# Optimization experiments

Hardware: AMD Instinct MI355X
Metric: run time of the kernel (lower is better)

Reference implementation:

```python
import jax, jax.numpy as jnp
import numpy as np

B, C_IN, N_NODES = 128, 64, 1024
N_TRIPLES = 3 * (N_NODES - 1)  # node 0 is the shared zero vector


def _btc(x, idx, w, b):
    # x: [B, C, N]; idx: [B, 3M]; w: [O, C, 3]; b: [O]
    Bv, C, _ = x.shape
    T = idx.shape[1]
    g = jnp.take_along_axis(x, jnp.broadcast_to(idx[:, None, :], (Bv, C, T)), axis=2)
    g = g.reshape(Bv, C, T // 3, 3)  # stride-3 kernel-3 conv == per-triple contraction
    out = jnp.einsum('bcnk,ock->bon', g, w) + b[None, :, None]
    zero = jnp.zeros((Bv, out.shape[1], 1), dtype=out.dtype)
    return jnp.concatenate([zero, out], axis=2)  # re-prepend zero node -> [B, O, N]


def _tln(x):
    mean = jnp.mean(x, axis=(1, 2), keepdims=True)
    std = jnp.std(x, axis=(1, 2), ddof=1, keepdims=True)  # torch.std is unbiased
    return (x - mean) / (std + 1e-5)


def _tower(x, idx, p):
    x = jax.nn.leaky_relu(_tln(_btc(x, idx, p['w_conv1'], p['b_conv1'])), 0.01)
    x = jax.nn.leaky_relu(_tln(_btc(x, idx, p['w_conv2'], p['b_conv2'])), 0.01)
    x = _tln(_btc(x, idx, p['w_conv3'], p['b_conv3']))
    x = jnp.max(x, axis=2)  # DynamicPooling -> [B, 64]
    x = jax.nn.leaky_relu(x @ p['w_fc1'].T + p['b_fc1'], 0.01)
    return x @ p['w_fc2'].T + p['b_fc2']  # [B, 1]  (Dropout is identity at eval)


def setup_inputs() -> dict:
    key = jax.random.key(0)
    ks = jax.random.split(key, 12)
    s = 0.05
    return {
        'data1': jax.random.normal(ks[0], (B, C_IN, N_NODES), jnp.float32),
        'idx1': jax.random.randint(ks[1], (B, N_TRIPLES, 1), 0, N_NODES, dtype=jnp.int64)
                if jax.config.jax_enable_x64 else
                jax.random.randint(ks[1], (B, N_TRIPLES, 1), 0, N_NODES).astype(jnp.int32),
        'data2': jax.random.normal(ks[2], (B, C_IN, N_NODES), jnp.float32),
        'idx2': jax.random.randint(ks[3], (B, N_TRIPLES, 1), 0, N_NODES).astype(jnp.int32),
        'w_conv1': jax.random.normal(ks[4], (256, C_IN, 3), jnp.float32) * s,
        'b_conv1': jnp.zeros((256,), jnp.float32),
        'w_conv2': jax.random.normal(ks[5], (128, 256, 3), jnp.float32) * s,
        'b_conv2': jnp.zeros((128,), jnp.float32),
        'w_conv3': jax.random.normal(ks[6], (64, 128, 3), jnp.float32) * s,
        'b_conv3': jnp.zeros((64,), jnp.float32),
        'w_fc1': jax.random.normal(ks[7], (32, 64), jnp.float32) * s,
        'b_fc1': jnp.zeros((32,), jnp.float32),
        'w_fc2': jax.random.normal(ks[8], (1, 32), jnp.float32) * s,
        'b_fc2': jnp.zeros((1,), jnp.float32),
    }


def reference(data1, idx1, data2, idx2,
              w_conv1, b_conv1, w_conv2, b_conv2, w_conv3, b_conv3,
              w_fc1, b_fc1, w_fc2, b_fc2):
    p = dict(w_conv1=w_conv1, b_conv1=b_conv1, w_conv2=w_conv2, b_conv2=b_conv2,
             w_conv3=w_conv3, b_conv3=b_conv3, w_fc1=w_fc1, b_fc1=b_fc1,
             w_fc2=w_fc2, b_fc2=b_fc2)
    y1 = _tower(data1, idx1[..., 0], p)
    y2 = _tower(data2, idx2[..., 0], p)
    return jnp.squeeze(jax.nn.sigmoid(y1 - y2), axis=1)  # [B]
```

## Files before the change

### kernel.cpp

```cpp
#include <hip/hip_runtime.h>
#include <math.h>

typedef __attribute__((ext_vector_type(8))) short short8;
typedef __attribute__((ext_vector_type(4))) float f32x4;
typedef __attribute__((ext_vector_type(2))) float f32x2;

#define LRELU(x) ((x) > 0.0f ? (x) : 0.01f * (x))

struct __align__(4) Int3 { int x, y, z; };

__device__ __forceinline__ unsigned short f2bf(float f) {
    unsigned int u = __float_as_uint(f);
    return (unsigned short)((u + 0x7FFFu + ((u >> 16) & 1u)) >> 16);
}
__device__ __forceinline__ unsigned int pack_bf16_pair(float lo, float hi) {
    unsigned int ul = __float_as_uint(lo) + 0x8000u;
    unsigned int uh = __float_as_uint(hi) + 0x8000u;
    return (ul >> 16) | (uh & 0xFFFF0000u);
}
__device__ __forceinline__ float2 stats_from(const float* sums, int b, float count) {
    float s = sums[2 * b], q = sums[2 * b + 1];
    float mean = s / count;
    float var = (q - s * s / count) / (count - 1.0f);
    var = fmaxf(var, 0.0f);
    return make_float2(mean, 1.0f / (sqrtf(var) + 1e-5f));
}
__device__ __forceinline__ void atomicMaxF(float* a, float v) {
    if (v >= 0.0f) atomicMax((int*)a, __float_as_int(v));
    else           atomicMin((unsigned int*)a, __float_as_uint(v));
}
__device__ __forceinline__ unsigned int fp8x4_nact(unsigned int u, float a, float c) {
    f32x2 lo = __builtin_amdgcn_cvt_pk_f32_fp8(u, false);
    f32x2 hi = __builtin_amdgcn_cvt_pk_f32_fp8(u, true);
    lo = lo * a + c; hi = hi * a + c;
    f32x2 ml = lo * 0.01f, mh = hi * 0.01f;
    lo = __builtin_elementwise_max(lo, ml);
    hi = __builtin_elementwise_max(hi, mh);
    int r = __builtin_amdgcn_cvt_pk_fp8_f32(lo.x, lo.y, 0, false);
    r = __builtin_amdgcn_cvt_pk_fp8_f32(hi.x, hi.y, r, true);
    return (unsigned int)r;
}
__device__ __forceinline__ int perm128(int o) {
    return ((o >> 6) << 6) | (((o >> 3) & 3) << 4) | (((o >> 5) & 1) << 3) | (o & 7);
}

template <int MT, int WM>
__device__ __forceinline__ void mfma_step(const unsigned short* wt, const unsigned short* gt,
                                          f32x4 (&acc)[MT][4],
                                          int wo, int wn, int quad, int l15, int blkid)
{
#pragma unroll
    for (int st = 0; st < 2; ++st) {
        short8 af[MT], bfv[4];
        const int qb = st * 4 + quad;
#pragma unroll
        for (int i = 0; i < MT; i++) {
            const int orow = wo * WM + i * 16 + l15;
            af[i] = *(const short8*)&wt[orow * 64 + ((qb ^ blkid) << 3)];
        }
#pragma unroll
        for (int t = 0; t < 4; t++) {
            const int nrow = wn * 64 + t * 16 + l15;
            bfv[t] = *(const short8*)&gt[nrow * 64 + ((qb ^ blkid) << 3)];
        }
#pragma unroll
        for (int i = 0; i < MT; i++)
#pragma unroll
            for (int t = 0; t < 4; t++)
                acc[i][t] = __builtin_amdgcn_mfma_f32_16x16x32_bf16(
                    af[i], bfv[t], acc[i][t], 0, 0, 0);
    }
}

__global__ void prep_all(const float* __restrict__ w1, unsigned short* __restrict__ wq1,
                         const float* __restrict__ w2, unsigned char* __restrict__ wq2,
                         const float* __restrict__ w3, unsigned char* __restrict__ wq3)
{
    const int tid = blockIdx.x * blockDim.x + threadIdx.x;
    const int stride = gridDim.x * blockDim.x;
    for (int i = tid; i < 256 * 192; i += stride) {
        int o = i / 192, kp = i - o * 192;
        int j = kp >> 6, c = kp & 63;
        wq1[i] = f2bf(w1[(o * 64 + c) * 3 + j]);
    }
    for (int i = tid; i < (128 * 768) >> 2; i += stride) {
        const int e0 = i << 2;
        const int o = e0 / 768, r0 = e0 - o * 768;
        const int kc = r0 >> 7, ro = r0 & 127;
        const int k0 = ((ro >> 6) << 6) + (((ro >> 3) & 1) << 5) + (((ro >> 4) & 3) << 3) + (ro & 7);
        const int kp0 = kc * 128 + k0;
        const int j = kp0 >> 8, c0 = kp0 & 255;
        const float* src = &w2[(o * 256 + c0) * 3 + j];
        float f0 = src[0], f1 = src[3], f2 = src[6], f3 = src[9];
        int r = __builtin_amdgcn_cvt_pk_fp8_f32(f0, f1, 0, false);
        r = __builtin_amdgcn_cvt_pk_fp8_f32(f2, f3, r, true);
        *(unsigned int*)&wq2[e0] = (unsigned int)r;
    }
    for (int i = tid; i < (64 * 384) >> 2; i += stride) {
        const int e0 = i << 2;
        const int o = e0 / 384, r0 = e0 - o * 384;
        const int kc = r0 >> 7, ro = r0 & 127;
        const int k0 = ((ro >> 6) << 6) + (((ro >> 3) & 1) << 5) + (((ro >> 4) & 3) << 3) + (ro & 7);
        const int kp0 = kc * 128 + k0;
        const int j = kp0 >> 7, c0 = kp0 & 127;
        const float* src = &w3[(o * 128 + c0) * 3 + j];
        float f0 = src[0], f1 = src[3], f2 = src[6], f3 = src[9];
        int r = __builtin_amdgcn_cvt_pk_fp8_f32(f0, f1, 0, false);
        r = __builtin_amdgcn_cvt_pk_fp8_f32(f2, f3, r, true);
        *(unsigned int*)&wq3[e0] = (unsigned int)r;
    }
}

__global__ __launch_bounds__(256) void transpose_in(const float* __restrict__ inA,
                                                    const float* __restrict__ inB,
                                                    unsigned short* __restrict__ xT,
                                                    float* __restrict__ sums,
                                                    unsigned int* __restrict__ pmax)
{
    const int b = blockIdx.y, n0 = blockIdx.x * 64;
    const float* in = (b >= 128 ? inB : inA) + ((size_t)(b & 127) * 64) * 1024;
    const int tid = threadIdx.x;
    if (blockIdx.x == 0 && blockIdx.y == 0) {
        const int nBv = gridDim.y;
        for (int i = tid; i < 3 * nBv * 2; i += 256) sums[i] = 0.0f;
        for (int i = tid; i < nBv * 64; i += 256) pmax[i] = 0xFFFFFFFFu;
    }
    __shared__ float tile[64][65];
    const int nn = tid & 63, cw = tid >> 6;
#pragma unroll
    for (int i = 0; i < 16; i++) {
        int c = i * 4 + cw;
        tile[c][nn] = in[(size_t)c * 1024 + n0 + nn];
    }
    __syncthreads();
    const int n = tid >> 2, cp = (tid & 3) * 16;
    unsigned int pk[8];
#pragma unroll
    for (int i = 0; i < 8; i++) {
        unsigned short lo = f2bf(tile[cp + 2 * i][n]);
        unsigned short hi = f2bf(tile[cp + 2 * i + 1][n]);
        pk[i] = (unsigned int)lo | ((unsigned int)hi << 16);
    }
    unsigned short* dst = xT + ((size_t)b * 1024 + n0 + n) * 64 + cp;
    uint4 v0 = {pk[0], pk[1], pk[2], pk[3]};
    uint4 v1 = {pk[4], pk[5], pk[6], pk[7]};
    *(uint4*)dst = v0;
    *(uint4*)(dst + 8) = v1;
}

__global__ __launch_bounds__(256) void norm_act_fp8(unsigned char* __restrict__ a,
                                                    const float* __restrict__ sums,
                                                    float count, int u4PerB)
{
    const int b = blockIdx.y;
    float2 st = stats_from(sums, b, count);
    const float na = st.y, nc = -st.x * st.y;
    uint4* p = (uint4*)a + (size_t)b * u4PerB;
    for (int idx = blockIdx.x * 256 + threadIdx.x; idx < u4PerB; idx += gridDim.x * 256) {
        uint4 v = p[idx];
        v.x = fp8x4_nact(v.x, na, nc);
        v.y = fp8x4_nact(v.y, na, nc);
        v.z = fp8x4_nact(v.z, na, nc);
        v.w = fp8x4_nact(v.w, na, nc);
        p[idx] = v;
    }
}

__global__ __launch_bounds__(256, 3) void conv1_mfma(
    const unsigned short* __restrict__ xT,
    const int* __restrict__ idxA,
    const int* __restrict__ idxB,
    const unsigned short* __restrict__ wq,
    const float* __restrict__ bias,
    unsigned char* __restrict__ out,
    float* __restrict__ sums)
{
    const int b   = blockIdx.x;
    const int o0  = blockIdx.y * 128;
    const int nt0 = blockIdx.z << 7;
    const int tid = threadIdx.x;
    const int lane = tid & 63, wave = tid >> 6;
    const int wo = wave & 1, wn = wave >> 1;
    const int quad = lane >> 4, l15 = lane & 15;
    const int blkid = lane & 7;

    __shared__ __align__(16) unsigned short wt[128 * 64];
    __shared__ __align__(16) unsigned short gt[128 * 64];

    f32x4 acc[4][4];
#pragma unroll
    for (int i = 0; i < 4; i++)
#pragma unroll
        for (int t = 0; t < 4; t++) acc[i][t] = (f32x4){0.f, 0.f, 0.f, 0.f};

    const unsigned short* xTb = xT + (((size_t)b) << 10) * 64;
    const int* idxb = (b >= 128 ? idxB : idxA) + (size_t)(b & 127) * 3069;

    const int gr = tid >> 1, gh = tid & 1;
    int s0, s1, s2;
    {
        int n = nt0 + gr;
        int t0 = (n == 0) ? 0 : (n - 1);
        const Int3 sv = *(const Int3*)&idxb[3 * t0];
        s0 = sv.x; s1 = sv.y; s2 = sv.z;
    }
    const int wr = tid >> 1, wseg = tid & 1;
    const unsigned short* wrow = wq + (size_t)(o0 + wr) * 192 + wseg * 32;
    const int gswz = gr & 7, wswz = wr & 7;

    uint4 g0A, g1A, g2A, g3A;
    uint4 g0B, g1B, g2B, g3B;

#define LOADC(S, KC) {                                                           \
        const int src_ = ((KC) == 0) ? s0 : (((KC) == 1) ? s1 : s2);             \
        const uint4* gp_ = (const uint4*)(xTb + (size_t)src_ * 64 + gh * 32);    \
        g0##S = gp_[0]; g1##S = gp_[1]; g2##S = gp_[2]; g3##S = gp_[3];          \
    }

#define STAGE(S, KC) {                                                           \
        const uint4* wp_ = (const uint4*)(wrow + ((KC) << 6));                   \
        uint4 wv0 = wp_[0], wv1 = wp_[1], wv2 = wp_[2], wv3 = wp_[3];            \
        *(uint4*)&gt[gr * 64 + (((gh << 2) | 0) ^ gswz) * 8] = g0##S;            \
        *(uint4*)&gt[gr * 64 + (((gh << 2) | 1) ^ gswz) * 8] = g1##S;            \
        *(uint4*)&gt[gr * 64 + (((gh << 2) | 2) ^ gswz) * 8] = g2##S;            \
        *(uint4*)&gt[gr * 64 + (((gh << 2) | 3) ^ gswz) * 8] = g3##S;            \
        *(uint4*)&wt[wr * 64 + ((wseg * 4 + 0) ^ wswz) * 8] = wv0;               \
        *(uint4*)&wt[wr * 64 + ((wseg * 4 + 1) ^ wswz) * 8] = wv1;               \
        *(uint4*)&wt[wr * 64 + ((wseg * 4 + 2) ^ wswz) * 8] = wv2;               \
        *(uint4*)&wt[wr * 64 + ((wseg * 4 + 3) ^ wswz) * 8] = wv3;               \
    }

    LOADC(A, 0);
    LOADC(B, 1);
    int kc = 0;
    for (; kc + 2 <= 3; kc += 2) {
        if (kc) __syncthreads();
        STAGE(A, kc);
        if (kc + 2 < 3) LOADC(A, kc + 2);
        __syncthreads();
        mfma_step<4, 64>(wt, gt, acc, wo, wn, quad, l15, blkid);
        __syncthreads();
        STAGE(B, kc + 1);
        __syncthreads();
        mfma_step<4, 64>(wt, gt, acc, wo, wn, quad, l15, blkid);
    }
    {
        __syncthreads();
        STAGE(A, 2);
        __syncthreads();
        mfma_step<4, 64>(wt, gt, acc, wo, wn, quad, l15, blkid);
    }
#undef LOADC
#undef STAGE

    __syncthreads();
    unsigned char* eb = (unsigned char*)gt;
    float lsum = 0.f, lsq = 0.f;
#pragma unroll
    for (int i = 0; i < 4; i++) {
        const int obl = wo * 64 + i * 16 + quad * 4;
        const int op  = perm128(obl);
        const float4 bv = *(const float4*)(bias + o0 + obl);
#pragma unroll
        for (int t = 0; t < 4; t++) {
            const int nl = wn * 64 + t * 16 + l15;
            float v0 = acc[i][t][0] + bv.x;
            float v1 = acc[i][t][1] + bv.y;
            float v2 = acc[i][t][2] + bv.z;
            float v3 = acc[i][t][3] + bv.w;
            if (nt0 + nl == 0) { v0 = v1 = v2 = v3 = 0.f; }
            lsum += v0 + v1 + v2 + v3;
            lsq  += v0 * v0 + v1 * v1 + v2 * v2 + v3 * v3;
            int r = __builtin_amdgcn_cvt_pk_fp8_f32(v0, v1, 0, false);
            r = __builtin_amdgcn_cvt_pk_fp8_f32(v2, v3, r, true);
            *(unsigned int*)&eb[nl * 128 + (op ^ ((nl & 7) << 4))] = (unsigned int)r;
        }
    }
#pragma unroll
    for (int off = 32; off > 0; off >>= 1) {
        lsum += __shfl_down(lsum, off);
        lsq  += __shfl_down(lsq, off);
    }
    float* red = (float*)wt;
    if (lane == 0) { red[wave] = lsum; red[4 + wave] = lsq; }
    __syncthreads();
#pragma unroll
    for (int c = 0; c < 4; ++c) {
        const int ch = c * 256 + tid;
        const int row = ch >> 3, off = (ch & 7) << 4;
        uint4 v = *(const uint4*)&eb[row * 128 + (off ^ ((row & 7) << 4))];
        *(uint4*)&out[((size_t)b * 1024 + nt0 + row) * 256 + o0 + off] = v;
    }
    if (tid == 0) {
        atomicAdd(&sums[2 * b + 0], red[0] + red[1] + red[2] + red[3]);
        atomicAdd(&sums[2 * b + 1], red[4] + red[5] + red[6] + red[7]);
    }
}

__global__ __launch_bounds__(256, 3) void conv2_fp8(
    const unsigned char* __restrict__ a1,
    const int* __restrict__ idxA,
    const int* __restrict__ idxB,
    const unsigned char* __restrict__ wq8,
    const float* __restrict__ bias,
    unsigned char* __restrict__ out,
    float* __restrict__ sums)
{
    const int b   = blockIdx.x;
    const int nt0 = blockIdx.z << 7;
    const int tid = threadIdx.x;
    const int lane = tid & 63, wave = tid >> 6;
    const int wo = wave & 1, wn = wave >> 1;
    const int quad = lane >> 4, l15 = lane & 15;
    const int blkid = lane & 7;

    __shared__ __align__(16) unsigned char wt8[128 * 128];
    __shared__ __align__(16) unsigned char gt8[128 * 128];

    f32x4 acc[4][4];
#pragma unroll
    for (int i = 0; i < 4; i++)
#pragma unroll
        for (int t = 0; t < 4; t++) acc[i][t] = (f32x4){0.f, 0.f, 0.f, 0.f};

    const unsigned char* xb = a1 + (((size_t)b) << 10) * 256;
    const int* idxb = (b >= 128 ? idxB : idxA) + (size_t)(b & 127) * 3069;

    const int gr = tid >> 1, gh = tid & 1;
    int si0, si1, si2;
    {
        int n = nt0 + gr;
        int t0 = (n == 0) ? 0 : (n - 1);
        const Int3 sv = *(const Int3*)&idxb[3 * t0];
        si0 = sv.x; si1 = sv.y; si2 = sv.z;
    }
    const unsigned char* wrow = wq8 + (size_t)gr * 768 + gh * 64;
    const int swz = gr & 7;

    uint4 g0A, g1A, g2A, g3A;
    uint4 g0B, g1B, g2B, g3B;

#define LOADC2(S, KC) {                                                          \
        const int j_  = (KC) >> 1;                                               \
        const int c0_ = ((KC) & 1) << 7;                                         \
        const int src_ = (j_ == 0) ? si0 : ((j_ == 1) ? si1 : si2);              \
        const uint4* gp_ = (const uint4*)(xb + (size_t)src_ * 256 + c0_ + gh * 64); \
        g0##S = gp_[0]; g1##S = gp_[1]; g2##S = gp_[2]; g3##S = gp_[3];          \
    }

#define STAGE2(S, KC) {                                                          \
        const uint4* wp_ = (const uint4*)(wrow + (KC) * 128);                    \
        uint4 wv0 = wp_[0], wv1 = wp_[1], wv2 = wp_[2], wv3 = wp_[3];            \
        *(uint4*)&gt8[gr * 128 + (((gh << 2) | 0) ^ swz) * 16] = g0##S;          \
        *(uint4*)&gt8[gr * 128 + (((gh << 2) | 1) ^ swz) * 16] = g1##S;          \
        *(uint4*)&gt8[gr * 128 + (((gh << 2) | 2) ^ swz) * 16] = g2##S;          \
        *(uint4*)&gt8[gr * 128 + (((gh << 2) | 3) ^ swz) * 16] = g3##S;          \
        *(uint4*)&wt8[gr * 128 + (((gh << 2) | 0) ^ swz) * 16] = wv0;            \
        *(uint4*)&wt8[gr * 128 + (((gh << 2) | 1) ^ swz) * 16] = wv1;            \
        *(uint4*)&wt8[gr * 128 + (((gh << 2) | 2) ^ swz) * 16] = wv2;            \
        *(uint4*)&wt8[gr * 128 + (((gh << 2) | 3) ^ swz) * 16] = wv3;            \
    }

#define MFMA_STEP2 {                                                             \
        _Pragma("unroll")                                                        \
        for (int pp = 0; pp < 2; ++pp) {                                         \
            ulonglong2 a0v, a1v, a2v, a3v, b0v, b1v, b2v, b3v;                   \
            {                                                                    \
                const int cx = (((pp * 4 + quad) ^ blkid) << 4);                 \
                a0v = *(const ulonglong2*)&wt8[(wo * 64 +  0 + l15) * 128 + cx]; \
                a1v = *(const ulonglong2*)&wt8[(wo * 64 + 16 + l15) * 128 + cx]; \
                a2v = *(const ulonglong2*)&wt8[(wo * 64 + 32 + l15) * 128 + cx]; \
                a3v = *(const ulonglong2*)&wt8[(wo * 64 + 48 + l15) * 128 + cx]; \
                b0v = *(const ulonglong2*)&gt8[(wn * 64 +  0 + l15) * 128 + cx]; \
                b1v = *(const ulonglong2*)&gt8[(wn * 64 + 16 + l15) * 128 + cx]; \
                b2v = *(const ulonglong2*)&gt8[(wn * 64 + 32 + l15) * 128 + cx]; \
                b3v = *(const ulonglong2*)&gt8[(wn * 64 + 48 + l15) * 128 + cx]; \
            }                                                                    \
            acc[0][0] = __builtin_amdgcn_mfma_f32_16x16x32_fp8_fp8((long)a0v.x, (long)b0v.x, acc[0][0], 0, 0, 0); \
            acc[0][1] = __builtin_amdgcn_mfma_f32_16x16x32_fp8_fp8((long)a0v.x, (long)b1v.x, acc[0][1], 0, 0, 0); \
            acc[0][2] = __builtin_amdgcn_mfma_f32_16x16x32_fp8_fp8((long)a0v.x, (long)b2v.x, acc[0][2], 0, 0, 0); \
            acc[0][3] = __builtin_amdgcn_mfma_f32_16x16x32_fp8_fp8((long)a0v.x, (long)b3v.x, acc[0][3], 0, 0, 0); \
            acc[1][0] = __builtin_amdgcn_mfma_f32_16x16x32_fp8_fp8((long)a1v.x, (long)b0v.x, acc[1][0], 0, 0, 0); \
            acc[1][1] = __builtin_amdgcn_mfma_f32_16x16x32_fp8_fp8((long)a1v.x, (long)b1v.x, acc[1][1], 0, 0, 0); \
            acc[1][2] = __builtin_amdgcn_mfma_f32_16x16x32_fp8_fp8((long)a1v.x, (long)b2v.x, acc[1][2], 0, 0, 0); \
            acc[1][3] = __builtin_amdgcn_mfma_f32_16x16x32_fp8_fp8((long)a1v.x, (long)b3v.x, acc[1][3], 0, 0, 0); \
            acc[2][0] = __builtin_amdgcn_mfma_f32_16x16x32_fp8_fp8((long)a2v.x, (long)b0v.x, acc[2][0], 0, 0, 0); \
            acc[2][1] = __builtin_amdgcn_mfma_f32_16x16x32_fp8_fp8((long)a2v.x, (long)b1v.x, acc[2][1], 0, 0, 0); \
            acc[2][2] = __builtin_amdgcn_mfma_f32_16x16x32_fp8_fp8((long)a2v.x, (long)b2v.x, acc[2][2], 0, 0, 0); \
            acc[2][3] = __builtin_amdgcn_mfma_f32_16x16x32_fp8_fp8((long)a2v.x, (long)b3v.x, acc[2][3], 0, 0, 0); \
            acc[3][0] = __builtin_amdgcn_mfma_f32_16x16x32_fp8_fp8((long)a3v.x, (long)b0v.x, acc[3][0], 0, 0, 0); \
            acc[3][1] = __builtin_amdgcn_mfma_f32_16x16x32_fp8_fp8((long)a3v.x, (long)b1v.x, acc[3][1], 0, 0, 0); \
            acc[3][2] = __builtin_amdgcn_mfma_f32_16x16x32_fp8_fp8((long)a3v.x, (long)b2v.x, acc[3][2], 0, 0, 0); \
            acc[3][3] = __builtin_amdgcn_mfma_f32_16x16x32_fp8_fp8((long)a3v.x, (long)b3v.x, acc[3][3], 0, 0, 0); \
            acc[0][0] = __builtin_amdgcn_mfma_f32_16x16x32_fp8_fp8((long)a0v.y, (long)b0v.y, acc[0][0], 0, 0, 0); \
            acc[0][1] = __builtin_amdgcn_mfma_f32_16x16x32_fp8_fp8((long)a0v.y, (long)b1v.y, acc[0][1], 0, 0, 0); \
            acc[0][2] = __builtin_amdgcn_mfma_f32_16x16x32_fp8_fp8((long)a0v.y, (long)b2v.y, acc[0][2], 0, 0, 0); \
            acc[0][3] = __builtin_amdgcn_mfma_f32_16x16x32_fp8_fp8((long)a0v.y, (long)b3v.y, acc[0][3], 0, 0, 0); \
            acc[1][0] = __builtin_amdgcn_mfma_f32_16x16x32_fp8_fp8((long)a1v.y, (long)b0v.y, acc[1][0], 0, 0, 0); \
            acc[1][1] = __builtin_amdgcn_mfma_f32_16x16x32_fp8_fp8((long)a1v.y, (long)b1v.y, acc[1][1], 0, 0, 0); \
            acc[1][2] = __builtin_amdgcn_mfma_f32_16x16x32_fp8_fp8((long)a1v.y, (long)b2v.y, acc[1][2], 0, 0, 0); \
            acc[1][3] = __builtin_amdgcn_mfma_f32_16x16x32_fp8_fp8((long)a1v.y, (long)b3v.y, acc[1][3], 0, 0, 0); \
            acc[2][0] = __builtin_amdgcn_mfma_f32_16x16x32_fp8_fp8((long)a2v.y, (long)b0v.y, acc[2][0], 0, 0, 0); \
            acc[2][1] = __builtin_amdgcn_mfma_f32_16x16x32_fp8_fp8((long)a2v.y, (long)b1v.y, acc[2][1], 0, 0, 0); \
            acc[2][2] = __builtin_amdgcn_mfma_f32_16x16x32_fp8_fp8((long)a2v.y, (long)b2v.y, acc[2][2], 0, 0, 0); \
            acc[2][3] = __builtin_amdgcn_mfma_f32_16x16x32_fp8_fp8((long)a2v.y, (long)b3v.y, acc[2][3], 0, 0, 0); \
            acc[3][0] = __builtin_amdgcn_mfma_f32_16x16x32_fp8_fp8((long)a3v.y, (long)b0v.y, acc[3][0], 0, 0, 0); \
            acc[3][1] = __builtin_amdgcn_mfma_f32_16x16x32_fp8_fp8((long)a3v.y, (long)b1v.y, acc[3][1], 0, 0, 0); \
            acc[3][2] = __builtin_amdgcn_mfma_f32_16x16x32_fp8_fp8((long)a3v.y, (long)b2v.y, acc[3][2], 0, 0, 0); \
            acc[3][3] = __builtin_amdgcn_mfma_f32_16x16x32_fp8_fp8((long)a3v.y, (long)b3v.y, acc[3][3], 0, 0, 0); \
        }                                                                        \
    }

    LOADC2(A, 0);
    LOADC2(B, 1);
    int kc = 0;
    for (; kc + 2 <= 6; kc += 2) {
        if (kc) __syncthreads();
        STAGE2(A, kc);
        if (kc + 2 < 6) LOADC2(A, kc + 2);
        __syncthreads();
        MFMA_STEP2;
        __syncthreads();
        STAGE2(B, kc + 1);
        if (kc + 3 < 6) LOADC2(B, kc + 3);
        __syncthreads();
        MFMA_STEP2;
    }
#undef LOADC2
#undef STAGE2
#undef MFMA_STEP2

    __syncthreads();
    unsigned char* eb = gt8;
    float lsum = 0.f, lsq = 0.f;
#pragma unroll
    for (int i = 0; i < 4; i++) {
        const int obl = wo * 64 + i * 16 + quad * 4;
        const int op  = perm128(obl);
        const float4 bv = *(const float4*)(bias + obl);
#pragma unroll
        for (int t = 0; t < 4; t++) {
            const int nl = wn * 64 + t * 16 + l15;
            float v0 = acc[i][t][0] + bv.x;
            float v1 = acc[i][t][1] + bv.y;
            float v2 = acc[i][t][2] + bv.z;
            float v3 = acc[i][t][3] + bv.w;
            if (nt0 + nl == 0) { v0 = v1 = v2 = v3 = 0.f; }
            lsum += v0 + v1 + v2 + v3;
            lsq  += v0 * v0 + v1 * v1 + v2 * v2 + v3 * v3;
            int r = __builtin_amdgcn_cvt_pk_fp8_f32(v0, v1, 0, false);
            r = __builtin_amdgcn_cvt_pk_fp8_f32(v2, v3, r, true);
            *(unsigned int*)&eb[nl * 128 + (op ^ ((nl & 7) << 4))] = (unsigned int)r;
        }
    }
#pragma unroll
    for (int off = 32; off > 0; off >>= 1) {
        lsum += __shfl_down(lsum, off);
        lsq  += __shfl_down(lsq, off);
    }
    float* red = (float*)wt8;
    if (lane == 0) { red[wave] = lsum; red[4 + wave] = lsq; }
    __syncthreads();
#pragma unroll
    for (int c = 0; c < 4; ++c) {
        const int ch = c * 256 + tid;
        const int row = ch >> 3, off = (ch & 7) << 4;
        uint4 v = *(const uint4*)&eb[row * 128 + (off ^ ((row & 7) << 4))];
        *(uint4*)&out[((size_t)b * 1024 + nt0 + row) * 128 + off] = v;
    }
    if (tid == 0) {
        atomicAdd(&sums[2 * b + 0], red[0] + red[1] + red[2] + red[3]);
        atomicAdd(&sums[2 * b + 1], red[4] + red[5] + red[6] + red[7]);
    }
}

__global__ __launch_bounds__(256, 3) void conv3_fp8(
    const unsigned char* __restrict__ a2,
    const int* __restrict__ idxA,
    const int* __restrict__ idxB,
    const unsigned char* __restrict__ wq8,
    const float* __restrict__ bias,
    float* __restrict__ sums,
    float* __restrict__ pmax)
{
    const int b   = blockIdx.x;
    const int nt0 = blockIdx.z << 7;
    const int tid = threadIdx.x;
    const int lane = tid & 63, wave = tid >> 6;
    const int wo = wave & 1, wn = wave >> 1;
    const int quad = lane >> 4, l15 = lane & 15;
    const int blkid = lane & 7;

    __shared__ __align__(16) unsigned char wt8[64 * 128];
    __shared__ __align__(16) unsigned char gt8[128 * 128];

    f32x4 acc[2][4];
#pragma unroll
    for (int i = 0; i < 2; i++)
#pragma unroll
        for (int t = 0; t < 4; t++) acc[i][t] = (f32x4){0.f, 0.f, 0.f, 0.f};

    const unsigned char* xb = a2 + (((size_t)b) << 10) * 128;
    const int* idxb = (b >= 128 ? idxB : idxA) + (size_t)(b & 127) * 3069;

    const int gr = tid >> 1, gh = tid & 1;
    int si0, si1, si2;
    {
        int n = nt0 + gr;
        int t0 = (n == 0) ? 0 : (n - 1);
        const Int3 sv = *(const Int3*)&idxb[3 * t0];
        si0 = sv.x; si1 = sv.y; si2 = sv.z;
    }
    const int wr = tid >> 2, wseg = tid & 3;
    const unsigned char* wrow = wq8 + (size_t)wr * 384 + wseg * 32;
    const int gswz = gr & 7, wswz = wr & 7;

    uint4 g0A, g1A, g2A, g3A;
    uint4 g0B, g1B, g2B, g3B;

#define LOADC3(S, KC) {                                                          \
        const int src_ = ((KC) == 0) ? si0 : (((KC) == 1) ? si1 : si2);          \
        const uint4* gp_ = (const uint4*)(xb + (size_t)src_ * 128 + gh * 64);    \
        g0##S = gp_[0]; g1##S = gp_[1]; g2##S = gp_[2]; g3##S = gp_[3];          \
    }

#define STAGE3(S, KC) {                                                          \
        const uint4* wp_ = (const uint4*)(wrow + (KC) * 128);                    \
        uint4 wv0 = wp_[0], wv1 = wp_[1];                                        \
        *(uint4*)&gt8[gr * 128 + (((gh << 2) | 0) ^ gswz) * 16] = g0##S;         \
        *(uint4*)&gt8[gr * 128 + (((gh << 2) | 1) ^ gswz) * 16] = g1##S;         \
        *(uint4*)&gt8[gr * 128 + (((gh << 2) | 2) ^ gswz) * 16] = g2##S;         \
        *(uint4*)&gt8[gr * 128 + (((gh << 2) | 3) ^ gswz) * 16] = g3##S;         \
        *(uint4*)&wt8[wr * 128 + (((wseg << 1) | 0) ^ wswz) * 16] = wv0;         \
        *(uint4*)&wt8[wr * 128 + (((wseg << 1) | 1) ^ wswz) * 16] = wv1;         \
    }

#define MFMA_STEP3 {                                                             \
        _Pragma("unroll")                                                        \
        for (int pp = 0; pp < 2; ++pp) {                                         \
            ulonglong2 a0v, a1v, b0v, b1v, b2v, b3v;                             \
            {                                                                    \
                const int cx = (((pp * 4 + quad) ^ blkid) << 4);                 \
                a0v = *(const ulonglong2*)&wt8[(wo * 32 +  0 + l15) * 128 + cx]; \
                a1v = *(const ulonglong2*)&wt8[(wo * 32 + 16 + l15) * 128 + cx]; \
                b0v = *(const ulonglong2*)&gt8[(wn * 64 +  0 + l15) * 128 + cx]; \
                b1v = *(const ulonglong2*)&gt8[(wn * 64 + 16 + l15) * 128 + cx]; \
                b2v = *(const ulonglong2*)&gt8[(wn * 64 + 32 + l15) * 128 + cx]; \
                b3v = *(const ulonglong2*)&gt8[(wn * 64 + 48 + l15) * 128 + cx]; \
            }                                                                    \
            acc[0][0] = __builtin_amdgcn_mfma_f32_16x16x32_fp8_fp8((long)a0v.x, (long)b0v.x, acc[0][0], 0, 0, 0); \
            acc[0][1] = __builtin_amdgcn_mfma_f32_16x16x32_fp8_fp8((long)a0v.x, (long)b1v.x, acc[0][1], 0, 0, 0); \
            acc[0][2] = __builtin_amdgcn_mfma_f32_16x16x32_fp8_fp8((long)a0v.x, (long)b2v.x, acc[0][2], 0, 0, 0); \
            acc[0][3] = __builtin_amdgcn_mfma_f32_16x16x32_fp8_fp8((long)a0v.x, (long)b3v.x, acc[0][3], 0, 0, 0); \
            acc[1][0] = __builtin_amdgcn_mfma_f32_16x16x32_fp8_fp8((long)a1v.x, (long)b0v.x, acc[1][0], 0, 0, 0); \
            acc[1][1] = __builtin_amdgcn_mfma_f32_16x16x32_fp8_fp8((long)a1v.x, (long)b1v.x, acc[1][1], 0, 0, 0); \
            acc[1][2] = __builtin_amdgcn_mfma_f32_16x16x32_fp8_fp8((long)a1v.x, (long)b2v.x, acc[1][2], 0, 0, 0); \
            acc[1][3] = __builtin_amdgcn_mfma_f32_16x16x32_fp8_fp8((long)a1v.x, (long)b3v.x, acc[1][3], 0, 0, 0); \
            acc[0][0] = __builtin_amdgcn_mfma_f32_16x16x32_fp8_fp8((long)a0v.y, (long)b0v.y, acc[0][0], 0, 0, 0); \
            acc[0][1] = __builtin_amdgcn_mfma_f32_16x16x32_fp8_fp8((long)a0v.y, (long)b1v.y, acc[0][1], 0, 0, 0); \
            acc[0][2] = __builtin_amdgcn_mfma_f32_16x16x32_fp8_fp8((long)a0v.y, (long)b2v.y, acc[0][2], 0, 0, 0); \
            acc[0][3] = __builtin_amdgcn_mfma_f32_16x16x32_fp8_fp8((long)a0v.y, (long)b3v.y, acc[0][3], 0, 0, 0); \
            acc[1][0] = __builtin_amdgcn_mfma_f32_16x16x32_fp8_fp8((long)a1v.y, (long)b0v.y, acc[1][0], 0, 0, 0); \
            acc[1][1] = __builtin_amdgcn_mfma_f32_16x16x32_fp8_fp8((long)a1v.y, (long)b1v.y, acc[1][1], 0, 0, 0); \
            acc[1][2] = __builtin_amdgcn_mfma_f32_16x16x32_fp8_fp8((long)a1v.y, (long)b2v.y, acc[1][2], 0, 0, 0); \
            acc[1][3] = __builtin_amdgcn_mfma_f32_16x16x32_fp8_fp8((long)a1v.y, (long)b3v.y, acc[1][3], 0, 0, 0); \
        }                                                                        \
    }

    LOADC3(A, 0);
    LOADC3(B, 1);
    int kc = 0;
    for (; kc + 2 <= 3; kc += 2) {
        if (kc) __syncthreads();
        STAGE3(A, kc);
        if (kc + 2 < 3) LOADC3(A, kc + 2);
        __syncthreads();
        MFMA_STEP3;
        __syncthreads();
        STAGE3(B, kc + 1);
        __syncthreads();
        MFMA_STEP3;
    }
    {
        __syncthreads();
        STAGE3(A, 2);
        __syncthreads();
        MFMA_STEP3;
    }
#undef LOADC3
#undef STAGE3
#undef MFMA_STEP3

    __syncthreads();
    float lsum = 0.f, lsq = 0.f;
#pragma unroll
    for (int i = 0; i < 2; i++) {
        const int ob = wo * 32 + i * 16 + quad * 4;
        const float4 bv = *(const float4*)(bias + ob);
        float mx0 = -1e30f, mx1 = -1e30f, mx2 = -1e30f, mx3 = -1e30f;
#pragma unroll
        for (int t = 0; t < 4; t++) {
            const int n = nt0 + wn * 64 + t * 16 + l15;
            float v0 = acc[i][t][0] + bv.x;
            float v1 = acc[i][t][1] + bv.y;
            float v2 = acc[i][t][2] + bv.z;
            float v3 = acc[i][t][3] + bv.w;
            if (n == 0) { v0 = v1 = v2 = v3 = 0.f; }
            lsum += v0 + v1 + v2 + v3;
            lsq  += v0 * v0 + v1 * v1 + v2 * v2 + v3 * v3;
            mx0 = fmaxf(mx0, v0); mx1 = fmaxf(mx1, v1);
            mx2 = fmaxf(mx2, v2); mx3 = fmaxf(mx3, v3);
        }
#pragma unroll
        for (int off = 1; off < 16; off <<= 1) {
            mx0 = fmaxf(mx0, __shfl_xor(mx0, off));
            mx1 = fmaxf(mx1, __shfl_xor(mx1, off));
            mx2 = fmaxf(mx2, __shfl_xor(mx2, off));
            mx3 = fmaxf(mx3, __shfl_xor(mx3, off));
        }
        if (l15 == 0) {
            atomicMaxF(&pmax[(size_t)b * 64 + ob + 0], mx0);
            atomicMaxF(&pmax[(size_t)b * 64 + ob + 1], mx1);
            atomicMaxF(&pmax[(size_t)b * 64 + ob + 2], mx2);
            atomicMaxF(&pmax[(size_t)b * 64 + ob + 3], mx3);
        }
    }
#pragma unroll
    for (int off = 32; off > 0; off >>= 1) {
        lsum += __shfl_down(lsum, off);
        lsq  += __shfl_down(lsq, off);
    }
    float* red = (float*)wt8;
    if (lane == 0) { red[wave] = lsum; red[4 + wave] = lsq; }
    __syncthreads();
    if (tid == 0) {
        atomicAdd(&sums[2 * b + 0], red[0] + red[1] + red[2] + red[3]);
        atomicAdd(&sums[2 * b + 1], red[4] + red[5] + red[6] + red[7]);
    }
}

__global__ __launch_bounds__(64) void fc_head(
    const float* __restrict__ pmax, const float* __restrict__ sums3, float count,
    const float* __restrict__ w_fc1, const float* __restrict__ b_fc1,
    const float* __restrict__ w_fc2, const float* __restrict__ b_fc2,
    float* __restrict__ y)
{
    const int b = blockIdx.x, t = threadIdx.x;
    __shared__ float pooled[64];
    __shared__ float hid[32];
    float2 s = stats_from(sums3, b, count);
    pooled[t] = (pmax[(size_t)b * 64 + t] - s.x) * s.y;
    __syncthreads();
    if (t < 32) {
        float h = b_fc1[t];
#pragma unroll
        for (int c = 0; c < 64; c++) h += pooled[c] * w_fc1[t * 64 + c];
        hid[t] = LRELU(h);
    }
    __syncthreads();
    if (t == 0) {
        float v = b_fc2[0];
#pragma unroll
        for (int c = 0; c < 32; c++) v += hid[c] * w_fc2[c];
        y[b] = v;
    }
}

__global__ void sigmoid_diff(const float* __restrict__ y1,
                             const float* __restrict__ y2,
                             float* __restrict__ out)
{
    int b = threadIdx.x;
    if (b < 128) out[b] = 1.0f / (1.0f + expf(-(y1[b] - y2[b])));
}

extern "C" void kernel_launch(void* const* d_in, const int* in_sizes, int n_in,
                              void* d_out, int out_size, void* d_ws, size_t ws_size,
                              hipStream_t stream)
{
    const float* data1 = (const float*)d_in[0];
    const int*   idx1  = (const int*)d_in[1];
    const float* data2 = (const float*)d_in[2];
    const int*   idx2  = (const int*)d_in[3];
    const float* w1 = (const float*)d_in[4];
    const float* b1 = (const float*)d_in[5];
    const float* w2 = (const float*)d_in[6];
    const float* b2 = (const float*)d_in[7];
    const float* w3 = (const float*)d_in[8];
    const float* b3 = (const float*)d_in[9];
    const float* wfc1 = (const float*)d_in[10];
    const float* bfc1 = (const float*)d_in[11];
    const float* wfc2 = (const float*)d_in[12];
    const float* bfc2 = (const float*)d_in[13];

    const size_t needM = (size_t)256 * 1024 * (64 * 2 + 256 * 1 + 128 * 1) + 768 * 1024;
    const bool merged = ws_size >= needM;
    const int nB = merged ? 256 : 128;
    const size_t szXT = (size_t)nB * 1024 * 64 * 2;
    const size_t szA1 = (size_t)nB * 1024 * 256;
    const size_t szA2 = (size_t)nB * 1024 * 128;

    char* ws = (char*)d_ws;
    unsigned short* xT = (unsigned short*)ws;
    unsigned char*  a1 = (unsigned char*)(ws + szXT);
    unsigned char*  a2 = (unsigned char*)(ws + szXT + szA1);
    char* tail = ws + szXT + szA1 + szA2;
    unsigned short* wq1   = (unsigned short*)tail;
    unsigned char*  wq2f8 = (unsigned char*)(tail + 128 * 1024);
    unsigned char*  wq3f8 = (unsigned char*)(tail + 384 * 1024);
    float* sums = (float*)(tail + 448 * 1024);
    float* pmax = (float*)(tail + 512 * 1024);
    float* yv   = (float*)(tail + 640 * 1024);

    prep_all<<<96, 256, 0, stream>>>(w1, wq1, w2, wq2f8, w3, wq3f8);

    const int nIter = merged ? 1 : 2;
    for (int t = 0; t < nIter; ++t) {
        const float* dA = (merged || t == 0) ? data1 : data2;
        const float* dB = merged ? data2 : dA;
        const int* iA = (merged || t == 0) ? idx1 : idx2;
        const int* iB = merged ? idx2 : iA;
        float* s1 = sums;
        float* s2 = sums + nB * 2;
        float* s3 = sums + nB * 4;

        transpose_in<<<dim3(16, nB), 256, 0, stream>>>(dA, dB, xT, sums,
                                                       (unsigned int*)pmax);

        conv1_mfma<<<dim3(nB, 2, 8), 256, 0, stream>>>(
            xT, iA, iB, wq1, b1, a1, s1);

        norm_act_fp8<<<dim3(16, nB), 256, 0, stream>>>(a1, s1, 256.0f * 1024.0f, 16384);

        conv2_fp8<<<dim3(nB, 1, 8), 256, 0, stream>>>(
            a1, iA, iB, wq2f8, b2, a2, s2);

        norm_act_fp8<<<dim3(8, nB), 256, 0, stream>>>(a2, s2, 128.0f * 1024.0f, 8192);

        conv3_fp8<<<dim3(nB, 1, 8), 256, 0, stream>>>(
            a2, iA, iB, wq3f8, b3, s3, pmax);

        fc_head<<<nB, 64, 0, stream>>>(pmax, s3, 64.0f * 1024.0f,
                                       wfc1, bfc1, wfc2, bfc2,
                                       yv + (merged ? 0 : t * 128));
    }
    sigmoid_diff<<<1, 128, 0, stream>>>(yv, yv + 128, (float*)d_out);
}
```

Measured before the change: 269.5 us.

## Switch conv1 input and weights from bf16 to fp8 MFMA

```diff
diff --git a/kernel.cpp b/kernel.cpp
--- a/kernel.cpp
+++ b/kernel.cpp
@@ -1,7 +1,6 @@
 #include <hip/hip_runtime.h>
 #include <math.h>
 
-typedef __attribute__((ext_vector_type(8))) short short8;
 typedef __attribute__((ext_vector_type(4))) float f32x4;
 typedef __attribute__((ext_vector_type(2))) float f32x2;
 
@@ -9,15 +8,6 @@
 
 struct __align__(4) Int3 { int x, y, z; };
 
-__device__ __forceinline__ unsigned short f2bf(float f) {
-    unsigned int u = __float_as_uint(f);
-    return (unsigned short)((u + 0x7FFFu + ((u >> 16) & 1u)) >> 16);
-}
-__device__ __forceinline__ unsigned int pack_bf16_pair(float lo, float hi) {
-    unsigned int ul = __float_as_uint(lo) + 0x8000u;
-    unsigned int uh = __float_as_uint(hi) + 0x8000u;
-    return (ul >> 16) | (uh & 0xFFFF0000u);
-}
 __device__ __forceinline__ float2 stats_from(const float* sums, int b, float count) {
     float s = sums[2 * b], q = sums[2 * b + 1];
     float mean = s / count;
@@ -44,44 +34,22 @@
     return ((o >> 6) << 6) | (((o >> 3) & 3) << 4) | (((o >> 5) & 1) << 3) | (o & 7);
 }
 
-template <int MT, int WM>
-__device__ __forceinline__ void mfma_step(const unsigned short* wt, const unsigned short* gt,
-                                          f32x4 (&acc)[MT][4],
-                                          int wo, int wn, int quad, int l15, int blkid)
-{
-#pragma unroll
-    for (int st = 0; st < 2; ++st) {
-        short8 af[MT], bfv[4];
-        const int qb = st * 4 + quad;
-#pragma unroll
-        for (int i = 0; i < MT; i++) {
-            const int orow = wo * WM + i * 16 + l15;
-            af[i] = *(const short8*)&wt[orow * 64 + ((qb ^ blkid) << 3)];
-        }
-#pragma unroll
-        for (int t = 0; t < 4; t++) {
-            const int nrow = wn * 64 + t * 16 + l15;
-            bfv[t] = *(const short8*)&gt[nrow * 64 + ((qb ^ blkid) << 3)];
-        }
-#pragma unroll
-        for (int i = 0; i < MT; i++)
-#pragma unroll
-            for (int t = 0; t < 4; t++)
-                acc[i][t] = __builtin_amdgcn_mfma_f32_16x16x32_bf16(
-                    af[i], bfv[t], acc[i][t], 0, 0, 0);
-    }
-}
-
-__global__ void prep_all(const float* __restrict__ w1, unsigned short* __restrict__ wq1,
+__global__ void prep_all(const float* __restrict__ w1, unsigned char* __restrict__ wq1,
                          const float* __restrict__ w2, unsigned char* __restrict__ wq2,
                          const float* __restrict__ w3, unsigned char* __restrict__ wq3)
 {
     const int tid = blockIdx.x * blockDim.x + threadIdx.x;
     const int stride = gridDim.x * blockDim.x;
-    for (int i = tid; i < 256 * 192; i += stride) {
-        int o = i / 192, kp = i - o * 192;
-        int j = kp >> 6, c = kp & 63;
-        wq1[i] = f2bf(w1[(o * 64 + c) * 3 + j]);
+    for (int i = tid; i < (256 * 192) >> 2; i += stride) {
+        const int e0 = i << 2;
+        const int o = e0 / 192, r0 = e0 - o * 192;
+        const int kc = r0 >> 6, p0 = r0 & 63;
+        const int k0 = (((p0 >> 3) & 1) << 5) + ((p0 >> 4) << 3) + (p0 & 7);
+        const float* src = &w1[(o * 64 + k0) * 3 + kc];
+        float f0 = src[0], f1 = src[3], f2 = src[6], f3 = src[9];
+        int r = __builtin_amdgcn_cvt_pk_fp8_f32(f0, f1, 0, false);
+        r = __builtin_amdgcn_cvt_pk_fp8_f32(f2, f3, r, true);
+        *(unsigned int*)&wq1[e0] = (unsigned int)r;
     }
     for (int i = tid; i < (128 * 768) >> 2; i += stride) {
         const int e0 = i << 2;
@@ -113,7 +81,7 @@
 
 __global__ __launch_bounds__(256) void transpose_in(const float* __restrict__ inA,
                                                     const float* __restrict__ inB,
-                                                    unsigned short* __restrict__ xT,
+                                                    unsigned char* __restrict__ xT8,
                                                     float* __restrict__ sums,
                                                     unsigned int* __restrict__ pmax)
 {
@@ -133,19 +101,35 @@
         tile[c][nn] = in[(size_t)c * 1024 + n0 + nn];
     }
     __syncthreads();
-    const int n = tid >> 2, cp = (tid & 3) * 16;
-    unsigned int pk[8];
-#pragma unroll
-    for (int i = 0; i < 8; i++) {
-        unsigned short lo = f2bf(tile[cp + 2 * i][n]);
-        unsigned short hi = f2bf(tile[cp + 2 * i + 1][n]);
-        pk[i] = (unsigned int)lo | ((unsigned int)hi << 16);
-    }
-    unsigned short* dst = xT + ((size_t)b * 1024 + n0 + n) * 64 + cp;
-    uint4 v0 = {pk[0], pk[1], pk[2], pk[3]};
-    uint4 v1 = {pk[4], pk[5], pk[6], pk[7]};
-    *(uint4*)dst = v0;
-    *(uint4*)(dst + 8) = v1;
+    const int n = tid >> 2, cg = tid & 3;
+    unsigned int u0, u1, u2, u3;
+    {
+        int k0 = cg * 8;
+        float f0 = tile[k0][n], f1 = tile[k0 + 1][n], f2 = tile[k0 + 2][n], f3 = tile[k0 + 3][n];
+        int r = __builtin_amdgcn_cvt_pk_fp8_f32(f0, f1, 0, false);
+        u0 = (unsigned int)__builtin_amdgcn_cvt_pk_fp8_f32(f2, f3, r, true);
+    }
+    {
+        int k0 = cg * 8 + 4;
+        float f0 = tile[k0][n], f1 = tile[k0 + 1][n], f2 = tile[k0 + 2][n], f3 = tile[k0 + 3][n];
+        int r = __builtin_amdgcn_cvt_pk_fp8_f32(f0, f1, 0, false);
+        u1 = (unsigned int)__builtin_amdgcn_cvt_pk_fp8_f32(f2, f3, r, true);
+    }
+    {
+        int k0 = 32 + cg * 8;
+        float f0 = tile[k0][n], f1 = tile[k0 + 1][n], f2 = tile[k0 + 2][n], f3 = tile[k0 + 3][n];
+        int r = __builtin_amdgcn_cvt_pk_fp8_f32(f0, f1, 0, false);
+        u2 = (unsigned int)__builtin_amdgcn_cvt_pk_fp8_f32(f2, f3, r, true);
+    }
+    {
+        int k0 = 32 + cg * 8 + 4;
+        float f0 = tile[k0][n], f1 = tile[k0 + 1][n], f2 = tile[k0 + 2][n], f3 = tile[k0 + 3][n];
+        int r = __builtin_amdgcn_cvt_pk_fp8_f32(f0, f1, 0, false);
+        u3 = (unsigned int)__builtin_amdgcn_cvt_pk_fp8_f32(f2, f3, r, true);
+    }
+    unsigned char* dst = xT8 + ((size_t)b * 1024 + n0 + n) * 64 + cg * 16;
+    uint4 v = {u0, u1, u2, u3};
+    *(uint4*)dst = v;
 }
 
 __global__ __launch_bounds__(256) void norm_act_fp8(unsigned char* __restrict__ a,
@@ -166,11 +150,11 @@
     }
 }
 
-__global__ __launch_bounds__(256, 3) void conv1_mfma(
-    const unsigned short* __restrict__ xT,
+__global__ __launch_bounds__(256, 3) void conv1_fp8(
+    const unsigned char* __restrict__ xT8,
     const int* __restrict__ idxA,
     const int* __restrict__ idxB,
-    const unsigned short* __restrict__ wq,
+    const unsigned char* __restrict__ wq8,
     const float* __restrict__ bias,
     unsigned char* __restrict__ out,
     float* __restrict__ sums)
@@ -184,8 +168,8 @@
     const int quad = lane >> 4, l15 = lane & 15;
     const int blkid = lane & 7;
 
-    __shared__ __align__(16) unsigned short wt[128 * 64];
-    __shared__ __align__(16) unsigned short gt[128 * 64];
+    __shared__ __align__(16) unsigned char wt8[128 * 128];
+    __shared__ __align__(16) unsigned char gt8[128 * 128];
 
     f32x4 acc[4][4];
 #pragma unroll
@@ -193,7 +177,7 @@
 #pragma unroll
         for (int t = 0; t < 4; t++) acc[i][t] = (f32x4){0.f, 0.f, 0.f, 0.f};
 
-    const unsigned short* xTb = xT + (((size_t)b) << 10) * 64;
+    const unsigned char* xb = xT8 + (((size_t)b) << 10) * 64;
     const int* idxb = (b >= 128 ? idxB : idxA) + (size_t)(b & 127) * 3069;
 
     const int gr = tid >> 1, gh = tid & 1;
@@ -204,57 +188,102 @@
         const Int3 sv = *(const Int3*)&idxb[3 * t0];
         s0 = sv.x; s1 = sv.y; s2 = sv.z;
     }
-    const int wr = tid >> 1, wseg = tid & 1;
-    const unsigned short* wrow = wq + (size_t)(o0 + wr) * 192 + wseg * 32;
-    const int gswz = gr & 7, wswz = wr & 7;
-
-    uint4 g0A, g1A, g2A, g3A;
-    uint4 g0B, g1B, g2B, g3B;
-
-#define LOADC(S, KC) {                                                           \
-        const int src_ = ((KC) == 0) ? s0 : (((KC) == 1) ? s1 : s2);             \
-        const uint4* gp_ = (const uint4*)(xTb + (size_t)src_ * 64 + gh * 32);    \
-        g0##S = gp_[0]; g1##S = gp_[1]; g2##S = gp_[2]; g3##S = gp_[3];          \
-    }
-
-#define STAGE(S, KC) {                                                           \
-        const uint4* wp_ = (const uint4*)(wrow + ((KC) << 6));                   \
-        uint4 wv0 = wp_[0], wv1 = wp_[1], wv2 = wp_[2], wv3 = wp_[3];            \
-        *(uint4*)&gt[gr * 64 + (((gh << 2) | 0) ^ gswz) * 8] = g0##S;            \
-        *(uint4*)&gt[gr * 64 + (((gh << 2) | 1) ^ gswz) * 8] = g1##S;            \
-        *(uint4*)&gt[gr * 64 + (((gh << 2) | 2) ^ gswz) * 8] = g2##S;            \
-        *(uint4*)&gt[gr * 64 + (((gh << 2) | 3) ^ gswz) * 8] = g3##S;            \
-        *(uint4*)&wt[wr * 64 + ((wseg * 4 + 0) ^ wswz) * 8] = wv0;               \
-        *(uint4*)&wt[wr * 64 + ((wseg * 4 + 1) ^ wswz) * 8] = wv1;               \
-        *(uint4*)&wt[wr * 64 + ((wseg * 4 + 2) ^ wswz) * 8] = wv2;               \
-        *(uint4*)&wt[wr * 64 + ((wseg * 4 + 3) ^ wswz) * 8] = wv3;               \
-    }
-
-    LOADC(A, 0);
-    LOADC(B, 1);
-    int kc = 0;
-    for (; kc + 2 <= 3; kc += 2) {
-        if (kc) __syncthreads();
-        STAGE(A, kc);
-        if (kc + 2 < 3) LOADC(A, kc + 2);
-        __syncthreads();
-        mfma_step<4, 64>(wt, gt, acc, wo, wn, quad, l15, blkid);
-        __syncthreads();
-        STAGE(B, kc + 1);
-        __syncthreads();
-        mfma_step<4, 64>(wt, gt, acc, wo, wn, quad, l15, blkid);
-    }
-    {
-        __syncthreads();
-        STAGE(A, 2);
-        __syncthreads();
-        mfma_step<4, 64>(wt, gt, acc, wo, wn, quad, l15, blkid);
-    }
-#undef LOADC
-#undef STAGE
-
-    __syncthreads();
-    unsigned char* eb = (unsigned char*)gt;
+    const unsigned char* wrow = wq8 + (size_t)(o0 + gr) * 192;
+    const int swz = gr & 7;
+
+    uint4 g0A, g1A, g2A, g3A, w0A, w1A, w2A, w3A;
+    uint4 g0B, g1B, g2B, g3B, w0B, w1B, w2B, w3B;
+
+    {
+        const int srcA = gh ? s1 : s0;
+        const uint4* gp = (const uint4*)(xb + (size_t)srcA * 64);
+        g0A = gp[0]; g1A = gp[1]; g2A = gp[2]; g3A = gp[3];
+        const uint4* wp = (const uint4*)(wrow + (gh << 6));
+        w0A = wp[0]; w1A = wp[1]; w2A = wp[2]; w3A = wp[3];
+    }
+    if (gh == 0) {
+        const uint4* gp = (const uint4*)(xb + (size_t)s2 * 64);
+        g0B = gp[0]; g1B = gp[1]; g2B = gp[2]; g3B = gp[3];
+        const uint4* wp = (const uint4*)(wrow + 128);
+        w0B = wp[0]; w1B = wp[1]; w2B = wp[2]; w3B = wp[3];
+    }
+
+    *(uint4*)&gt8[gr * 128 + (((gh << 2) | 0) ^ swz) * 16] = g0A;
+    *(uint4*)&gt8[gr * 128 + (((gh << 2) | 1) ^ swz) * 16] = g1A;
+    *(uint4*)&gt8[gr * 128 + (((gh << 2) | 2) ^ swz) * 16] = g2A;
+    *(uint4*)&gt8[gr * 128 + (((gh << 2) | 3) ^ swz) * 16] = g3A;
+    *(uint4*)&wt8[gr * 128 + (((gh << 2) | 0) ^ swz) * 16] = w0A;
+    *(uint4*)&wt8[gr * 128 + (((gh << 2) | 1) ^ swz) * 16] = w1A;
+    *(uint4*)&wt8[gr * 128 + (((gh << 2) | 2) ^ swz) * 16] = w2A;
+    *(uint4*)&wt8[gr * 128 + (((gh << 2) | 3) ^ swz) * 16] = w3A;
+
+#define MFMA_PP(PP) {                                                            \
+        ulonglong2 a0v, a1v, a2v, a3v, b0v, b1v, b2v, b3v;                       \
+        {                                                                        \
+            const int cx = ((((PP) * 4 + quad) ^ blkid) << 4);                   \
+            a0v = *(const ulonglong2*)&wt8[(wo * 64 +  0 + l15) * 128 + cx];     \
+            a1v = *(const ulonglong2*)&wt8[(wo * 64 + 16 + l15) * 128 + cx];     \
+            a2v = *(const ulonglong2*)&wt8[(wo * 64 + 32 + l15) * 128 + cx];     \
+            a3v = *(const ulonglong2*)&wt8[(wo * 64 + 48 + l15) * 128 + cx];     \
+            b0v = *(const ulonglong2*)&gt8[(wn * 64 +  0 + l15) * 128 + cx];     \
+            b1v = *(const ulonglong2*)&gt8[(wn * 64 + 16 + l15) * 128 + cx];     \
+            b2v = *(const ulonglong2*)&gt8[(wn * 64 + 32 + l15) * 128 + cx];     \
+            b3v = *(const ulonglong2*)&gt8[(wn * 64 + 48 + l15) * 128 + cx];     \
+        }                                                                        \
+        acc[0][0] = __builtin_amdgcn_mfma_f32_16x16x32_fp8_fp8((long)a0v.x, (long)b0v.x, acc[0][0], 0, 0, 0); \
+        acc[0][1] = __builtin_amdgcn_mfma_f32_16x16x32_fp8_fp8((long)a0v.x, (long)b1v.x, acc[0][1], 0, 0, 0); \
+        acc[0][2] = __builtin_amdgcn_mfma_f32_16x16x32_fp8_fp8((long)a0v.x, (long)b2v.x, acc[0][2], 0, 0, 0); \
+        acc[0][3] = __builtin_amdgcn_mfma_f32_16x16x32_fp8_fp8((long)a0v.x, (long)b3v.x, acc[0][3], 0, 0, 0); \
+        acc[1][0] = __builtin_amdgcn_mfma_f32_16x16x32_fp8_fp8((long)a1v.x, (long)b0v.x, acc[1][0], 0, 0, 0); \
+        acc[1][1] = __builtin_amdgcn_mfma_f32_16x16x32_fp8_fp8((long)a1v.x, (long)b1v.x, acc[1][1], 0, 0, 0); \
+        acc[1][2] = __builtin_amdgcn_mfma_f32_16x16x32_fp8_fp8((long)a1v.x, (long)b2v.x, acc[1][2], 0, 0, 0); \
+        acc[1][3] = __builtin_amdgcn_mfma_f32_16x16x32_fp8_fp8((long)a1v.x, (long)b3v.x, acc[1][3], 0, 0, 0); \
+        acc[2][0] = __builtin_amdgcn_mfma_f32_16x16x32_fp8_fp8((long)a2v.x, (long)b0v.x, acc[2][0], 0, 0, 0); \
+        acc[2][1] = __builtin_amdgcn_mfma_f32_16x16x32_fp8_fp8((long)a2v.x, (long)b1v.x, acc[2][1], 0, 0, 0); \
+        acc[2][2] = __builtin_amdgcn_mfma_f32_16x16x32_fp8_fp8((long)a2v.x, (long)b2v.x, acc[2][2], 0, 0, 0); \
+        acc[2][3] = __builtin_amdgcn_mfma_f32_16x16x32_fp8_fp8((long)a2v.x, (long)b3v.x, acc[2][3], 0, 0, 0); \
+        acc[3][0] = __builtin_amdgcn_mfma_f32_16x16x32_fp8_fp8((long)a3v.x, (long)b0v.x, acc[3][0], 0, 0, 0); \
+        acc[3][1] = __builtin_amdgcn_mfma_f32_16x16x32_fp8_fp8((long)a3v.x, (long)b1v.x, acc[3][1], 0, 0, 0); \
+        acc[3][2] = __builtin_amdgcn_mfma_f32_16x16x32_fp8_fp8((long)a3v.x, (long)b2v.x, acc[3][2], 0, 0, 0); \
+        acc[3][3] = __builtin_amdgcn_mfma_f32_16x16x32_fp8_fp8((long)a3v.x, (long)b3v.x, acc[3][3], 0, 0, 0); \
+        acc[0][0] = __builtin_amdgcn_mfma_f32_16x16x32_fp8_fp8((long)a0v.y, (long)b0v.y, acc[0][0], 0, 0, 0); \
+        acc[0][1] = __builtin_amdgcn_mfma_f32_16x16x32_fp8_fp8((long)a0v.y, (long)b1v.y, acc[0][1], 0, 0, 0); \
+        acc[0][2] = __builtin_amdgcn_mfma_f32_16x16x32_fp8_fp8((long)a0v.y, (long)b2v.y, acc[0][2], 0, 0, 0); \
+        acc[0][3] = __builtin_amdgcn_mfma_f32_16x16x32_fp8_fp8((long)a0v.y, (long)b3v.y, acc[0][3], 0, 0, 0); \
+        acc[1][0] = __builtin_amdgcn_mfma_f32_16x16x32_fp8_fp8((long)a1v.y, (long)b0v.y, acc[1][0], 0, 0, 0); \
+        acc[1][1] = __builtin_amdgcn_mfma_f32_16x16x32_fp8_fp8((long)a1v.y, (long)b1v.y, acc[1][1], 0, 0, 0); \
+        acc[1][2] = __builtin_amdgcn_mfma_f32_16x16x32_fp8_fp8((long)a1v.y, (long)b2v.y, acc[1][2], 0, 0, 0); \
+        acc[1][3] = __builtin_amdgcn_mfma_f32_16x16x32_fp8_fp8((long)a1v.y, (long)b3v.y, acc[1][3], 0, 0, 0); \
+        acc[2][0] = __builtin_amdgcn_mfma_f32_16x16x32_fp8_fp8((long)a2v.y, (long)b0v.y, acc[2][0], 0, 0, 0); \
+        acc[2][1] = __builtin_amdgcn_mfma_f32_16x16x32_fp8_fp8((long)a2v.y, (long)b1v.y, acc[2][1], 0, 0, 0); \
+        acc[2][2] = __builtin_amdgcn_mfma_f32_16x16x32_fp8_fp8((long)a2v.y, (long)b2v.y, acc[2][2], 0, 0, 0); \
+        acc[2][3] = __builtin_amdgcn_mfma_f32_16x16x32_fp8_fp8((long)a2v.y, (long)b3v.y, acc[2][3], 0, 0, 0); \
+        acc[3][0] = __builtin_amdgcn_mfma_f32_16x16x32_fp8_fp8((long)a3v.y, (long)b0v.y, acc[3][0], 0, 0, 0); \
+        acc[3][1] = __builtin_amdgcn_mfma_f32_16x16x32_fp8_fp8((long)a3v.y, (long)b1v.y, acc[3][1], 0, 0, 0); \
+        acc[3][2] = __builtin_amdgcn_mfma_f32_16x16x32_fp8_fp8((long)a3v.y, (long)b2v.y, acc[3][2], 0, 0, 0); \
+        acc[3][3] = __builtin_amdgcn_mfma_f32_16x16x32_fp8_fp8((long)a3v.y, (long)b3v.y, acc[3][3], 0, 0, 0); \
+    }
+
+    __syncthreads();
+    MFMA_PP(0);
+    MFMA_PP(1);
+    __syncthreads();
+    if (gh == 0) {
+        *(uint4*)&gt8[gr * 128 + ((0 ^ swz) * 16)] = g0B;
+        *(uint4*)&gt8[gr * 128 + ((1 ^ swz) * 16)] = g1B;
+        *(uint4*)&gt8[gr * 128 + ((2 ^ swz) * 16)] = g2B;
+        *(uint4*)&gt8[gr * 128 + ((3 ^ swz) * 16)] = g3B;
+        *(uint4*)&wt8[gr * 128 + ((0 ^ swz) * 16)] = w0B;
+        *(uint4*)&wt8[gr * 128 + ((1 ^ swz) * 16)] = w1B;
+        *(uint4*)&wt8[gr * 128 + ((2 ^ swz) * 16)] = w2B;
+        *(uint4*)&wt8[gr * 128 + ((3 ^ swz) * 16)] = w3B;
+    }
+    __syncthreads();
+    MFMA_PP(0);
+#undef MFMA_PP
+
+    __syncthreads();
+    unsigned char* eb = gt8;
     float lsum = 0.f, lsq = 0.f;
 #pragma unroll
     for (int i = 0; i < 4; i++) {
@@ -281,7 +310,7 @@
         lsum += __shfl_down(lsum, off);
         lsq  += __shfl_down(lsq, off);
     }
-    float* red = (float*)wt;
+    float* red = (float*)wt8;
     if (lane == 0) { red[wave] = lsum; red[4 + wave] = lsq; }
     __syncthreads();
 #pragma unroll
@@ -693,26 +722,26 @@
     const float* wfc2 = (const float*)d_in[12];
     const float* bfc2 = (const float*)d_in[13];
 
-    const size_t needM = (size_t)256 * 1024 * (64 * 2 + 256 * 1 + 128 * 1) + 768 * 1024;
+    const size_t needM = (size_t)256 * 1024 * (64 + 256 + 128) + 768 * 1024;
     const bool merged = ws_size >= needM;
     const int nB = merged ? 256 : 128;
-    const size_t szXT = (size_t)nB * 1024 * 64 * 2;
+    const size_t szXT = (size_t)nB * 1024 * 64;
     const size_t szA1 = (size_t)nB * 1024 * 256;
     const size_t szA2 = (size_t)nB * 1024 * 128;
 
     char* ws = (char*)d_ws;
-    unsigned short* xT = (unsigned short*)ws;
-    unsigned char*  a1 = (unsigned char*)(ws + szXT);
-    unsigned char*  a2 = (unsigned char*)(ws + szXT + szA1);
+    unsigned char* xT8 = (unsigned char*)ws;
+    unsigned char* a1  = (unsigned char*)(ws + szXT);
+    unsigned char* a2  = (unsigned char*)(ws + szXT + szA1);
     char* tail = ws + szXT + szA1 + szA2;
-    unsigned short* wq1   = (unsigned short*)tail;
-    unsigned char*  wq2f8 = (unsigned char*)(tail + 128 * 1024);
-    unsigned char*  wq3f8 = (unsigned char*)(tail + 384 * 1024);
+    unsigned char* wq1f8 = (unsigned char*)tail;
+    unsigned char* wq2f8 = (unsigned char*)(tail + 128 * 1024);
+    unsigned char* wq3f8 = (unsigned char*)(tail + 384 * 1024);
     float* sums = (float*)(tail + 448 * 1024);
     float* pmax = (float*)(tail + 512 * 1024);
     float* yv   = (float*)(tail + 640 * 1024);
 
-    prep_all<<<96, 256, 0, stream>>>(w1, wq1, w2, wq2f8, w3, wq3f8);
+    prep_all<<<96, 256, 0, stream>>>(w1, wq1f8, w2, wq2f8, w3, wq3f8);
 
     const int nIter = merged ? 1 : 2;
     for (int t = 0; t < nIter; ++t) {
@@ -724,11 +753,11 @@
         float* s2 = sums + nB * 2;
         float* s3 = sums + nB * 4;
 
-        transpose_in<<<dim3(16, nB), 256, 0, stream>>>(dA, dB, xT, sums,
+        transpose_in<<<dim3(16, nB), 256, 0, stream>>>(dA, dB, xT8, sums,
                                                        (unsigned int*)pmax);
 
-        conv1_mfma<<<dim3(nB, 2, 8), 256, 0, stream>>>(
-            xT, iA, iB, wq1, b1, a1, s1);
+        conv1_fp8<<<dim3(nB, 2, 8), 256, 0, stream>>>(
+            xT8, iA, iB, wq1f8, b1, a1, s1);
 
         norm_act_fp8<<<dim3(16, nB), 256, 0, stream>>>(a1, s1, 256.0f * 1024.0f, 16384);
 
```

Measured after the change: 263.9 us (median of 2 runs). -2.1%, faster.
